# Kernel optimization log

Measured on AMD Instinct MI355X. Metric: run time of the kernel, lower is better.

The kernel has to match this reference:

```python
import jax, jax.numpy as jnp
import numpy as np

B, T, C = 4, 2048, 1024
H = 16
D = C // H  # head_dim = 64


def setup_inputs() -> dict:
    key = jax.random.key(0)
    k1, k2, k3 = jax.random.split(key, 3)
    x = jax.random.normal(k1, (B, T, C), dtype=jnp.float32)
    w_qkv = jax.random.normal(k2, (C, 3 * C), dtype=jnp.float32) * (C ** -0.5)
    b_qkv = jnp.zeros((3 * C,), dtype=jnp.float32)
    w_proj = jax.random.normal(k3, (C, C), dtype=jnp.float32) * (C ** -0.5)
    b_proj = jnp.zeros((C,), dtype=jnp.float32)
    return {"x": x, "w_qkv": w_qkv, "b_qkv": b_qkv, "w_proj": w_proj, "b_proj": b_proj}


def reference(x, w_qkv, b_qkv, w_proj, b_proj):
    # qkv projection: (B,T,C) -> (B,T,3,H,D) -> q,k,v each (B,H,T,D)
    qkv = (x @ w_qkv + b_qkv).reshape(B, T, 3, H, D)
    q, k, v = jnp.moveaxis(qkv, 2, 0)           # each (B, T, H, D)
    q = q.transpose(0, 2, 1, 3)                 # (B, H, T, D)
    k = k.transpose(0, 2, 1, 3)
    v = v.transpose(0, 2, 1, 3)

    scale = 1.0 / jnp.sqrt(jnp.float32(D))
    attn = jnp.einsum('bhqd,bhkd->bhqk', q, k) * scale  # (B,H,T,T)
    causal = jnp.tril(jnp.ones((T, T), dtype=bool))
    attn = jnp.where(causal[None, None], attn, -jnp.inf)
    attn = jax.nn.softmax(attn, axis=-1)
    # dropout p=0.0 (eval mode) -> identity
    out = jnp.einsum('bhqk,bhkd->bhqd', attn, v)        # (B,H,T,D)
    out = out.transpose(0, 2, 1, 3).reshape(B, T, C)
    return out @ w_proj + b_proj
```

## Files before the change

kernel.cpp:

```cpp
#include <hip/hip_runtime.h>
#include <hip/hip_bf16.h>


#define Bsz 4
#define Tsz 2048
#define Csz 1024
#define Hn  16
#define Dh  64

typedef unsigned short u16;
typedef __attribute__((ext_vector_type(8))) short bf16x8;
typedef __attribute__((ext_vector_type(4))) float f32x4;
typedef __attribute__((ext_vector_type(4))) unsigned int u32x4;
typedef __attribute__((ext_vector_type(2))) unsigned int u32x2;

__device__ __forceinline__ u16 f2b(float f) {
  __hip_bfloat16 h = __float2bfloat16(f);
  return *reinterpret_cast<u16*>(&h);
}

__device__ __forceinline__ unsigned pk2(float lo, float hi) {
  return __builtin_amdgcn_perm(__float_as_uint(hi) + 0x8000u,
                               __float_as_uint(lo) + 0x8000u, 0x07060302u);
}

#if __has_builtin(__builtin_amdgcn_exp2f)
#define EX2(x) __builtin_amdgcn_exp2f(x)
#else
#define EX2(x) exp2f(x)
#endif

__device__ __forceinline__ void gld_lds16(const void* g, void* lds) {
  __builtin_amdgcn_global_load_lds(
      (const __attribute__((address_space(1))) unsigned int*)g,
      (__attribute__((address_space(3))) unsigned int*)lds, 16, 0, 0);
}

__global__ __launch_bounds__(256) void prep(const float* __restrict__ x,
                                            u16* __restrict__ Xb,
                                            const float* __restrict__ w_qkv,
                                            u16* __restrict__ WqkvT,
                                            const float* __restrict__ w_proj,
                                            u16* __restrict__ WprojT) {
  const int bid = blockIdx.x;
  const int tid = threadIdx.x;
  if (bid < 4096) {
    size_t i = ((size_t)bid * 256 + tid) * 8;
    f32x4 a = *(const f32x4*)(x + i);
    f32x4 b = *(const f32x4*)(x + i + 4);
    u16 r[8];
#pragma unroll
    for (int j = 0; j < 4; ++j) { r[j] = f2b(a[j]); r[4 + j] = f2b(b[j]); }
    *(u32x4*)(Xb + i) = *(const u32x4*)r;
    return;
  }
  __shared__ u16 tile[64 * 66];
  const float* in;
  u16* out;
  int R, C, bx, by;
  int t = bid - 4096;
  if (t < 768) {
    in = w_qkv; out = WqkvT; R = 1024; C = 3072;
    bx = t & 15; by = t >> 4;
  } else {
    t -= 768;
    in = w_proj; out = WprojT; R = 1024; C = 1024;
    bx = t & 15; by = t >> 4;
  }
  const int r0 = bx * 64, c0 = by * 64;
#pragma unroll
  for (int i = 0; i < 16; ++i) {
    int idx = i * 256 + tid;
    int r = idx >> 6, c = idx & 63;
    tile[r * 66 + c] = f2b(in[(size_t)(r0 + r) * C + (c0 + c)]);
  }
  __syncthreads();
#pragma unroll
  for (int i = 0; i < 16; ++i) {
    int idx = i * 256 + tid;
    int c = idx >> 6, r = idx & 63;
    out[(size_t)(c0 + c) * R + (r0 + r)] = tile[r * 66 + c];
  }
}

__device__ __forceinline__ void gemm_tile_acc(const u16* __restrict__ A,
                                              const u16* __restrict__ Bt,
                                              int m0, int n0,
                                              u16* Als, u16* Bls,
                                              f32x4 acc[4][2]) {
  const int tid = threadIdx.x;
  const int w = tid >> 6, lane = tid & 63;
  const int wm = w & 1, wn = w >> 1;
  const int col = lane & 15, quad = lane >> 4;
#pragma unroll
  for (int mt = 0; mt < 4; ++mt)
#pragma unroll
    for (int nt = 0; nt < 2; ++nt)
      acc[mt][nt] = (f32x4){0.f, 0.f, 0.f, 0.f};

  const u16* asrc[2];
  const u16* bsrc[2];
#pragma unroll
  for (int c = 0; c < 2; ++c) {
    int slot = c * 512 + tid;
    int trow = slot >> 3, seg = slot & 7;
    size_t off = (size_t)trow * 1024 + (size_t)((seg ^ (trow & 7)) * 8);
    asrc[c] = A + (size_t)m0 * 1024 + off;
    bsrc[c] = Bt + (size_t)n0 * 1024 + off;
  }
  const int swz = col & 7;
  const int o0 = ((0 + quad) ^ swz) * 8;
  const int o1 = ((4 + quad) ^ swz) * 8;

#pragma unroll
  for (int c = 0; c < 2; ++c) {
    gld_lds16(asrc[c], (char*)Als + (size_t)(c * 512 + w * 64) * 16);
    gld_lds16(bsrc[c], (char*)Bls + (size_t)(c * 512 + w * 64) * 16);
    asrc[c] += 64; bsrc[c] += 64;
  }

  const int nkt = 1024 / 64;
  for (int t = 0; t < nkt; ++t) {
    asm volatile("s_waitcnt vmcnt(0)" ::: "memory");
    __builtin_amdgcn_s_barrier();
    __builtin_amdgcn_sched_barrier(0);
    const int cur = t & 1;
    if (t + 1 < nkt) {
      const int nxt = cur ^ 1;
      u16* Ad = Als + nxt * 8192;
      u16* Bd = Bls + nxt * 8192;
#pragma unroll
      for (int c = 0; c < 2; ++c) {
        gld_lds16(asrc[c], (char*)Ad + (size_t)(c * 512 + w * 64) * 16);
        gld_lds16(bsrc[c], (char*)Bd + (size_t)(c * 512 + w * 64) * 16);
        asrc[c] += 64; bsrc[c] += 64;
      }
    }
    const u16* Ac = Als + cur * 8192;
    const u16* Bc = Bls + cur * 8192;
    bf16x8 af[4][2], bfr[2][2];
#pragma unroll
    for (int mt = 0; mt < 4; ++mt) {
      const u16* r = Ac + (size_t)(wm * 64 + mt * 16 + col) * 64;
      af[mt][0] = *(const bf16x8*)(r + o0);
      af[mt][1] = *(const bf16x8*)(r + o1);
    }
#pragma unroll
    for (int nt = 0; nt < 2; ++nt) {
      const u16* r = Bc + (size_t)(wn * 32 + nt * 16 + col) * 64;
      bfr[nt][0] = *(const bf16x8*)(r + o0);
      bfr[nt][1] = *(const bf16x8*)(r + o1);
    }
#pragma unroll
    for (int kk = 0; kk < 2; ++kk)
#pragma unroll
      for (int mt = 0; mt < 4; ++mt)
#pragma unroll
        for (int nt = 0; nt < 2; ++nt)
          acc[mt][nt] = __builtin_amdgcn_mfma_f32_16x16x32_bf16(
              af[mt][kk], bfr[nt][kk], acc[mt][nt], 0, 0, 0);
  }
}

__global__ __launch_bounds__(512, 4) void gemm_qkv(const u16* __restrict__ X,
                                                   const u16* __restrict__ WT,
                                                   const float* __restrict__ bias,
                                                   u16* __restrict__ Q,
                                                   u16* __restrict__ Kc,
                                                   u16* __restrict__ Vt) {
  __shared__ __align__(16) u16 Als[2 * 128 * 64];
  __shared__ __align__(16) u16 Bls[2 * 128 * 64];
  f32x4 acc[4][2];
  const int m0 = blockIdx.x * 128, n0 = blockIdx.y * 128;
  gemm_tile_acc(X, WT, m0, n0, Als, Bls, acc);

  const float qscale = 0.18033688011112042f;
  const int tid = threadIdx.x;
  const int w = tid >> 6, lane = tid & 63;
  const int wm = w & 1, wn = w >> 1;
  const int col = lane & 15, quad = lane >> 4;
#pragma unroll
  for (int mt = 0; mt < 4; ++mt)
#pragma unroll
    for (int nt = 0; nt < 2; ++nt) {
      int n = n0 + wn * 32 + nt * 16 + col;
      int s = n >> 10, hh = (n >> 6) & (Hn - 1), d = n & 63;
      int mBase = m0 + wm * 64 + mt * 16 + quad * 4;
      int b = mBase >> 11, t0 = mBase & (Tsz - 1);
      if (s == 2) {
        u16 vals[4];
#pragma unroll
        for (int r = 0; r < 4; ++r) vals[r] = f2b(acc[mt][nt][r] + bias[n]);
        *(u32x2*)(Vt + ((size_t)(b * Hn + hh) * Dh + d) * Tsz + t0) =
            *(const u32x2*)vals;
      } else {
        const float scl = (s == 0) ? qscale : 1.f;
        u16* dst = (s == 0) ? Q : Kc;
#pragma unroll
        for (int r = 0; r < 4; ++r)
          dst[((size_t)(b * Hn + hh) * Tsz + (t0 + r)) * Dh + d] =
              f2b((acc[mt][nt][r] + bias[n]) * scl);
      }
    }
}

__global__ __launch_bounds__(512, 4) void gemm_proj(const u16* __restrict__ O,
                                                    const u16* __restrict__ WT,
                                                    const float* __restrict__ bias,
                                                    float* __restrict__ out) {
  __shared__ __align__(16) u16 Als[2 * 128 * 64];
  __shared__ __align__(16) u16 Bls[2 * 128 * 64];
  f32x4 acc[4][2];
  const int m0 = blockIdx.x * 128, n0 = blockIdx.y * 128;
  gemm_tile_acc(O, WT, m0, n0, Als, Bls, acc);

  const int tid = threadIdx.x;
  const int w = tid >> 6, lane = tid & 63;
  const int wm = w & 1, wn = w >> 1;
  const int col = lane & 15, quad = lane >> 4;
#pragma unroll
  for (int mt = 0; mt < 4; ++mt)
#pragma unroll
    for (int nt = 0; nt < 2; ++nt)
#pragma unroll
      for (int r = 0; r < 4; ++r) {
        int m = m0 + wm * 64 + mt * 16 + quad * 4 + r;
        int n = n0 + wn * 32 + nt * 16 + col;
        out[(size_t)m * Csz + n] = acc[mt][nt][r] + bias[n];
      }
}

__device__ __forceinline__ void attn_tile_stage(
    const u16* __restrict__ Kc, const u16* __restrict__ Vc,
    const bf16x8* aq, f32x4* oacc, float* lsum,
    bool domask, int rel, int qg, int col, int quad, int off0, int off1) {
  f32x4 sacc[4];
#pragma unroll
  for (int kt = 0; kt < 4; ++kt) sacc[kt] = (f32x4){0.f, 0.f, 0.f, 0.f};
#pragma unroll
  for (int ks = 0; ks < 2; ++ks)
#pragma unroll
    for (int kt = 0; kt < 4; ++kt) {
      bf16x8 bk = *(const bf16x8*)(&Kc[(kt * 16 + col) * 64 + (ks ? off1 : off0)]);
      sacc[kt] = __builtin_amdgcn_mfma_f32_16x16x32_bf16(bk, aq[ks],
                                                         sacc[kt], 0, 0, 0);
    }

  float e[4][4];
  if (domask) {
#pragma unroll
    for (int kt = 0; kt < 4; ++kt)
#pragma unroll
      for (int r = 0; r < 4; ++r) {
        int kl = rel + kt * 16 + quad * 4 + r;
        float p = (kl > qg) ? 0.f : EX2(sacc[kt][r]);
        lsum[kt] += p;
        e[kt][r] = p;
      }
  } else {
#pragma unroll
    for (int kt = 0; kt < 4; ++kt)
#pragma unroll
      for (int r = 0; r < 4; ++r) {
        float p = EX2(sacc[kt][r]);
        lsum[kt] += p;
        e[kt][r] = p;
      }
  }

#pragma unroll
  for (int ksg = 0; ksg < 2; ++ksg) {
    unsigned w00 = pk2(e[2 * ksg][0], e[2 * ksg][1]);
    unsigned w01 = pk2(e[2 * ksg][2], e[2 * ksg][3]);
    unsigned w10 = pk2(e[2 * ksg + 1][0], e[2 * ksg + 1][1]);
    unsigned w11 = pk2(e[2 * ksg + 1][2], e[2 * ksg + 1][3]);
    auto ra = __builtin_amdgcn_permlane32_swap(w00, w10, false, false);
    auto rb = __builtin_amdgcn_permlane32_swap(w01, w11, false, false);
    auto sa = __builtin_amdgcn_permlane16_swap(ra[0], ra[1], false, false);
    auto sb = __builtin_amdgcn_permlane16_swap(rb[0], rb[1], false, false);
    union { unsigned u[4]; bf16x8 v; } pf;
    pf.u[0] = sa[0]; pf.u[1] = sb[0]; pf.u[2] = sa[1]; pf.u[3] = sb[1];
#pragma unroll
    for (int dt = 0; dt < 4; ++dt) {
      bf16x8 bv = *(const bf16x8*)(&Vc[(dt * 16 + col) * 64 + (ksg ? off1 : off0)]);
      oacc[dt] = __builtin_amdgcn_mfma_f32_16x16x32_bf16(bv, pf.v,
                                                         oacc[dt], 0, 0, 0);
    }
  }
}

__global__ __launch_bounds__(512, 4) void attn(const u16* __restrict__ Q,
                                               const u16* __restrict__ Kg,
                                               const u16* __restrict__ Vt,
                                               u16* __restrict__ O) {
  __shared__ __align__(16) u16 Ks[3][64 * 64];
  __shared__ __align__(16) u16 Vs[3][64 * 64];

  const int d0 = blockIdx.x;
  const int xcd = d0 & 7;
  const int idx = d0 >> 3;
  const int bh = ((idx & 7) << 3) | xcd;
  const int a = idx >> 3;
  const int qlo = a, qhi = 15 - a;
  const int h = bh & (Hn - 1), b = bh >> 4;

  const int tid = threadIdx.x, w = tid >> 6, lane = tid & 63;
  const int col = lane & 15, quad = lane >> 4;
  const int qbl = qlo << 7, qbh = qhi << 7;

  const u16* Kbase = Kg + (size_t)bh * Tsz * Dh;
  const u16* Vbase = Vt + (size_t)bh * Dh * Tsz;

  const int trow = tid >> 3;
  const int xseg = ((tid & 7) ^ (trow & 7)) * 8;
  const size_t koff = (size_t)trow * 64 + xseg;
  const size_t voff = (size_t)trow * Tsz + xseg;
  const int swz = col & 7;
  const int off0 = ((0 + quad) ^ swz) << 3;
  const int off1 = ((4 + quad) ^ swz) << 3;

  bf16x8 aq_hi[2], aq_lo[2];
  {
    const u16* Qh = Q + ((size_t)bh * Tsz + qbh) * Dh;
    const u16* Ql = Q + ((size_t)bh * Tsz + qbl) * Dh;
#pragma unroll
    for (int ks = 0; ks < 2; ++ks) {
      aq_hi[ks] = *(const bf16x8*)(Qh + (size_t)(w * 16 + col) * Dh + ks * 32 + quad * 8);
      aq_lo[ks] = *(const bf16x8*)(Ql + (size_t)(w * 16 + col) * Dh + ks * 32 + quad * 8);
    }
  }
  asm volatile("s_waitcnt vmcnt(0)" ::: "memory");

  const int nst = 2 * qhi + 2;
  gld_lds16(Kbase + koff, &Ks[0][w * 512]);
  gld_lds16(Vbase + voff, &Vs[0][w * 512]);
  gld_lds16(Kbase + 4096 + koff, &Ks[1][w * 512]);
  gld_lds16(Vbase + 64 + voff, &Vs[1][w * 512]);

  f32x4 oacc_hi[4], oacc_lo[4];
#pragma unroll
  for (int dt = 0; dt < 4; ++dt) {
    oacc_hi[dt] = (f32x4){0.f, 0.f, 0.f, 0.f};
    oacc_lo[dt] = (f32x4){0.f, 0.f, 0.f, 0.f};
  }
  float lsum_hi[4] = {0.f, 0.f, 0.f, 0.f};
  float lsum_lo[4] = {0.f, 0.f, 0.f, 0.f};

  const u16* kdma = Kbase + 2 * 4096 + koff;
  const u16* vdma = Vbase + 2 * 64 + voff;

  const int qg = w * 16 + col;
  const int wge4 = (w >= 4) ? 1 : 0;
  const int smask_hi = 2 * qhi + wge4;
  const int smask_lo = 2 * qlo + wge4;
  const int lo_end = 2 * qlo + 1 + wge4;
  const int hi2 = 2 * qhi, lo2 = 2 * qlo;

  int cur = 0;
  for (int s = 0; s < nst; ++s) {
    if (s + 1 < nst) {
      asm volatile("s_waitcnt vmcnt(2)" ::: "memory");
    } else {
      asm volatile("s_waitcnt vmcnt(0)" ::: "memory");
    }
    __builtin_amdgcn_s_barrier();
    __builtin_amdgcn_sched_barrier(0);
    if (s + 2 < nst) {
      int pf = cur + 2; if (pf >= 3) pf -= 3;
      gld_lds16(kdma, &Ks[pf][w * 512]);
      gld_lds16(vdma, &Vs[pf][w * 512]);
      kdma += 4096;
      vdma += 64;
    }
    const u16* Kc = &Ks[cur][0];
    const u16* Vc = &Vs[cur][0];

    if (w >= 4 || s < nst - 1)
      attn_tile_stage(Kc, Vc, aq_hi, oacc_hi, lsum_hi,
                      s >= smask_hi, (s - hi2) * 64, qg, col, quad, off0, off1);
    if (s < lo_end)
      attn_tile_stage(Kc, Vc, aq_lo, oacc_lo, lsum_lo,
                      s >= smask_lo, (s - lo2) * 64, qg, col, quad, off0, off1);

    cur += 1; if (cur >= 3) cur = 0;
  }

  float vh = (lsum_hi[0] + lsum_hi[1]) + (lsum_hi[2] + lsum_hi[3]);
  vh += __shfl_xor(vh, 16);
  vh += __shfl_xor(vh, 32);
  const float invh = 1.0f / vh;
  float vl = (lsum_lo[0] + lsum_lo[1]) + (lsum_lo[2] + lsum_lo[3]);
  vl += __shfl_xor(vl, 16);
  vl += __shfl_xor(vl, 32);
  const float invl = 1.0f / vl;

  const int rgh = qbh + w * 16 + col;
  const int rgl = qbl + w * 16 + col;
  u16* OrowH = O + (((size_t)b * Tsz + rgh) * Hn + h) * Dh;
  u16* OrowL = O + (((size_t)b * Tsz + rgl) * Hn + h) * Dh;
#pragma unroll
  for (int dt = 0; dt < 4; ++dt) {
    u16 vh4[4], vl4[4];
#pragma unroll
    for (int r = 0; r < 4; ++r) {
      vh4[r] = f2b(oacc_hi[dt][r] * invh);
      vl4[r] = f2b(oacc_lo[dt][r] * invl);
    }
    *(u32x2*)(OrowH + dt * 16 + quad * 4) = *(const u32x2*)vh4;
    *(u32x2*)(OrowL + dt * 16 + quad * 4) = *(const u32x2*)vl4;
  }
}

extern "C" void kernel_launch(void* const* d_in, const int* in_sizes, int n_in,
                              void* d_out, int out_size, void* d_ws, size_t ws_size,
                              hipStream_t stream) {
  const float* x      = (const float*)d_in[0];
  const float* w_qkv  = (const float*)d_in[1];
  const float* b_qkv  = (const float*)d_in[2];
  const float* w_proj = (const float*)d_in[3];
  const float* b_proj = (const float*)d_in[4];
  float* out = (float*)d_out;

  u16* Xb     = (u16*)d_ws;
  u16* WqkvT  = Xb + (size_t)8192 * 1024;
  u16* WprojT = WqkvT + (size_t)3072 * 1024;
  u16* Qb     = WprojT + (size_t)1024 * 1024;
  u16* Kb     = Qb + (size_t)8192 * 1024;
  u16* Ob     = Kb + (size_t)8192 * 1024;
  u16* Vtb    = (u16*)d_out;

  prep<<<5120, 256, 0, stream>>>(x, Xb, w_qkv, WqkvT, w_proj, WprojT);
  gemm_qkv<<<dim3(64, 24), 512, 0, stream>>>(Xb, WqkvT, b_qkv, Qb, Kb, Vtb);
  attn<<<dim3(512), 512, 0, stream>>>(Qb, Kb, Vtb, Ob);
  gemm_proj<<<dim3(64, 8), 512, 0, stream>>>(Ob, WprojT, b_proj, out);
}
```

Measured before the change: 229.2 us.

## Use 256x256 block tiles for the QKV projection GEMM

Adds a new GEMM core that computes 256x256 output tiles per 512-thread block, with each wave holding an 8x4 grid of MFMA accumulators, and switches the QKV projection to it with a 32x12 grid. Larger tiles raise arithmetic intensity and cut global/LDS load traffic per FLOP. The cost is higher register and LDS use (64KB of double-buffered LDS), lower occupancy (launch bounds 2), and only 384 blocks, which is close to a single wave across the CUs and may leave some underused.

```diff
diff --git a/kernel.cpp b/kernel.cpp
--- a/kernel.cpp
+++ b/kernel.cpp
@@ -83,6 +83,122 @@
   }
 }
 
+__device__ __forceinline__ void gemm256_core(const u16* __restrict__ A,
+                                             const u16* __restrict__ Bt,
+                                             int m0, int n0,
+                                             u16* Als, u16* Bls,
+                                             f32x4 acc[8][4]) {
+  const int tid = threadIdx.x;
+  const int w = tid >> 6, lane = tid & 63;
+  const int wm = w & 1, wn = w >> 1;
+  const int col = lane & 15, quad = lane >> 4;
+#pragma unroll
+  for (int mt = 0; mt < 8; ++mt)
+#pragma unroll
+    for (int nt = 0; nt < 4; ++nt)
+      acc[mt][nt] = (f32x4){0.f, 0.f, 0.f, 0.f};
+
+  const u16* aP[4];
+  const u16* bP[4];
+#pragma unroll
+  for (int c = 0; c < 4; ++c) {
+    int slot = c * 512 + tid;
+    int trow = slot >> 3, seg = slot & 7;
+    size_t off = (size_t)trow * 1024 + (size_t)((seg ^ (trow & 7)) * 8);
+    aP[c] = A + (size_t)m0 * 1024 + off;
+    bP[c] = Bt + (size_t)n0 * 1024 + off;
+  }
+  const int swz = col & 7;
+  const int o0 = ((0 + quad) ^ swz) * 8;
+  const int o1 = ((4 + quad) ^ swz) * 8;
+
+#pragma unroll
+  for (int c = 0; c < 4; ++c) {
+    gld_lds16(aP[c], Als + c * 4096 + w * 512);
+    gld_lds16(bP[c], Bls + c * 4096 + w * 512);
+    aP[c] += 64; bP[c] += 64;
+  }
+
+  const int nkt = 1024 / 64;
+  for (int t = 0; t < nkt; ++t) {
+    asm volatile("s_waitcnt vmcnt(0)" ::: "memory");
+    __builtin_amdgcn_s_barrier();
+    __builtin_amdgcn_sched_barrier(0);
+    const int cur = t & 1;
+    if (t + 1 < nkt) {
+      const int nxt = cur ^ 1;
+      u16* Ad = Als + nxt * 16384;
+      u16* Bd = Bls + nxt * 16384;
+#pragma unroll
+      for (int c = 0; c < 4; ++c) {
+        gld_lds16(aP[c], Ad + c * 4096 + w * 512);
+        gld_lds16(bP[c], Bd + c * 4096 + w * 512);
+        aP[c] += 64; bP[c] += 64;
+      }
+    }
+    const u16* Ac = Als + cur * 16384;
+    const u16* Bc = Bls + cur * 16384;
+#pragma unroll
+    for (int ks = 0; ks < 2; ++ks) {
+      const int oo = ks ? o1 : o0;
+      bf16x8 bf[4];
+#pragma unroll
+      for (int nt = 0; nt < 4; ++nt)
+        bf[nt] = *(const bf16x8*)(Bc + (size_t)(wn * 64 + nt * 16 + col) * 64 + oo);
+#pragma unroll
+      for (int mt = 0; mt < 8; ++mt) {
+        bf16x8 af = *(const bf16x8*)(Ac + (size_t)(wm * 128 + mt * 16 + col) * 64 + oo);
+#pragma unroll
+        for (int nt = 0; nt < 4; ++nt)
+          acc[mt][nt] = __builtin_amdgcn_mfma_f32_16x16x32_bf16(af, bf[nt],
+                                                                acc[mt][nt], 0, 0, 0);
+      }
+    }
+  }
+}
+
+__global__ __launch_bounds__(512, 2) void gemm_qkv(const u16* __restrict__ X,
+                                                   const u16* __restrict__ WT,
+                                                   const float* __restrict__ bias,
+                                                   u16* __restrict__ Q,
+                                                   u16* __restrict__ Kc,
+                                                   u16* __restrict__ Vt) {
+  __shared__ __align__(16) u16 Als[2 * 256 * 64];
+  __shared__ __align__(16) u16 Bls[2 * 256 * 64];
+  f32x4 acc[8][4];
+  const int m0 = blockIdx.x * 256, n0 = blockIdx.y * 256;
+  gemm256_core(X, WT, m0, n0, Als, Bls, acc);
+
+  const float qscale = 0.18033688011112042f;
+  const int tid = threadIdx.x;
+  const int w = tid >> 6, lane = tid & 63;
+  const int wm = w & 1, wn = w >> 1;
+  const int col = lane & 15, quad = lane >> 4;
+#pragma unroll
+  for (int mt = 0; mt < 8; ++mt)
+#pragma unroll
+    for (int nt = 0; nt < 4; ++nt) {
+      int n = n0 + wn * 64 + nt * 16 + col;
+      int s = n >> 10, hh = (n >> 6) & (Hn - 1), d = n & 63;
+      int mBase = m0 + wm * 128 + mt * 16 + quad * 4;
+      int b = mBase >> 11, t0 = mBase & (Tsz - 1);
+      if (s == 2) {
+        u16 vals[4];
+#pragma unroll
+        for (int r = 0; r < 4; ++r) vals[r] = f2b(acc[mt][nt][r] + bias[n]);
+        *(u32x2*)(Vt + ((size_t)(b * Hn + hh) * Dh + d) * Tsz + t0) =
+            *(const u32x2*)vals;
+      } else {
+        const float scl = (s == 0) ? qscale : 1.f;
+        u16* dst = (s == 0) ? Q : Kc;
+#pragma unroll
+        for (int r = 0; r < 4; ++r)
+          dst[((size_t)(b * Hn + hh) * Tsz + (t0 + r)) * Dh + d] =
+              f2b((acc[mt][nt][r] + bias[n]) * scl);
+      }
+    }
+}
+
 __device__ __forceinline__ void gemm_tile_acc(const u16* __restrict__ A,
                                               const u16* __restrict__ Bt,
                                               int m0, int n0,
@@ -160,48 +276,6 @@
           acc[mt][nt] = __builtin_amdgcn_mfma_f32_16x16x32_bf16(
               af[mt][kk], bfr[nt][kk], acc[mt][nt], 0, 0, 0);
   }
-}
-
-__global__ __launch_bounds__(512, 4) void gemm_qkv(const u16* __restrict__ X,
-                                                   const u16* __restrict__ WT,
-                                                   const float* __restrict__ bias,
-                                                   u16* __restrict__ Q,
-                                                   u16* __restrict__ Kc,
-                                                   u16* __restrict__ Vt) {
-  __shared__ __align__(16) u16 Als[2 * 128 * 64];
-  __shared__ __align__(16) u16 Bls[2 * 128 * 64];
-  f32x4 acc[4][2];
-  const int m0 = blockIdx.x * 128, n0 = blockIdx.y * 128;
-  gemm_tile_acc(X, WT, m0, n0, Als, Bls, acc);
-
-  const float qscale = 0.18033688011112042f;
-  const int tid = threadIdx.x;
-  const int w = tid >> 6, lane = tid & 63;
-  const int wm = w & 1, wn = w >> 1;
-  const int col = lane & 15, quad = lane >> 4;
-#pragma unroll
-  for (int mt = 0; mt < 4; ++mt)
-#pragma unroll
-    for (int nt = 0; nt < 2; ++nt) {
-      int n = n0 + wn * 32 + nt * 16 + col;
-      int s = n >> 10, hh = (n >> 6) & (Hn - 1), d = n & 63;
-      int mBase = m0 + wm * 64 + mt * 16 + quad * 4;
-      int b = mBase >> 11, t0 = mBase & (Tsz - 1);
-      if (s == 2) {
-        u16 vals[4];
-#pragma unroll
-        for (int r = 0; r < 4; ++r) vals[r] = f2b(acc[mt][nt][r] + bias[n]);
-        *(u32x2*)(Vt + ((size_t)(b * Hn + hh) * Dh + d) * Tsz + t0) =
-            *(const u32x2*)vals;
-      } else {
-        const float scl = (s == 0) ? qscale : 1.f;
-        u16* dst = (s == 0) ? Q : Kc;
-#pragma unroll
-        for (int r = 0; r < 4; ++r)
-          dst[((size_t)(b * Hn + hh) * Tsz + (t0 + r)) * Dh + d] =
-              f2b((acc[mt][nt][r] + bias[n]) * scl);
-      }
-    }
 }
 
 __global__ __launch_bounds__(512, 4) void gemm_proj(const u16* __restrict__ O,
@@ -430,7 +504,7 @@
   u16* Vtb    = (u16*)d_out;
 
   prep<<<5120, 256, 0, stream>>>(x, Xb, w_qkv, WqkvT, w_proj, WprojT);
-  gemm_qkv<<<dim3(64, 24), 512, 0, stream>>>(Xb, WqkvT, b_qkv, Qb, Kb, Vtb);
+  gemm_qkv<<<dim3(32, 12), 512, 0, stream>>>(Xb, WqkvT, b_qkv, Qb, Kb, Vtb);
   attn<<<dim3(512), 512, 0, stream>>>(Qb, Kb, Vtb, Ob);
   gemm_proj<<<dim3(64, 8), 512, 0, stream>>>(Ob, WprojT, b_proj, out);
 }
```

Measured after the change: 243.4 us. +6.2%, slower.

## Load GEMM B operand directly from global into registers, drop B LDS staging

Applied to the files above, without the earlier changes.

The shared GEMM tile routine no longer stages the B (weight) tile through LDS. Each wave now reads its B fragments straight from global memory into registers every k-step. The change also halves shared memory per block and raises the launch-bounds occupancy hint from 4 to 6 for both QKV and projection GEMMs. This removes LDS traffic and footprint, but adds uncoalesced, unprefetched global loads on the critical path, and the wave pairs that share B columns now each fetch them separately.

```diff
diff --git a/kernel.cpp b/kernel.cpp
--- a/kernel.cpp
+++ b/kernel.cpp
@@ -86,7 +86,7 @@
 __device__ __forceinline__ void gemm_tile_acc(const u16* __restrict__ A,
                                               const u16* __restrict__ Bt,
                                               int m0, int n0,
-                                              u16* Als, u16* Bls,
+                                              u16* Als,
                                               f32x4 acc[4][2]) {
   const int tid = threadIdx.x;
   const int w = tid >> 6, lane = tid & 63;
@@ -99,24 +99,25 @@
       acc[mt][nt] = (f32x4){0.f, 0.f, 0.f, 0.f};
 
   const u16* asrc[2];
-  const u16* bsrc[2];
 #pragma unroll
   for (int c = 0; c < 2; ++c) {
     int slot = c * 512 + tid;
     int trow = slot >> 3, seg = slot & 7;
-    size_t off = (size_t)trow * 1024 + (size_t)((seg ^ (trow & 7)) * 8);
-    asrc[c] = A + (size_t)m0 * 1024 + off;
-    bsrc[c] = Bt + (size_t)n0 * 1024 + off;
+    asrc[c] = A + (size_t)m0 * 1024 + (size_t)trow * 1024 +
+              (size_t)((seg ^ (trow & 7)) * 8);
   }
   const int swz = col & 7;
   const int o0 = ((0 + quad) ^ swz) * 8;
   const int o1 = ((4 + quad) ^ swz) * 8;
 
+  const u16* bg[2];
+  bg[0] = Bt + (size_t)(n0 + wn * 32 + col) * 1024 + quad * 8;
+  bg[1] = Bt + (size_t)(n0 + wn * 32 + 16 + col) * 1024 + quad * 8;
+
 #pragma unroll
   for (int c = 0; c < 2; ++c) {
     gld_lds16(asrc[c], (char*)Als + (size_t)(c * 512 + w * 64) * 16);
-    gld_lds16(bsrc[c], (char*)Bls + (size_t)(c * 512 + w * 64) * 16);
-    asrc[c] += 64; bsrc[c] += 64;
+    asrc[c] += 64;
   }
 
   const int nkt = 1024 / 64;
@@ -128,17 +129,20 @@
     if (t + 1 < nkt) {
       const int nxt = cur ^ 1;
       u16* Ad = Als + nxt * 8192;
-      u16* Bd = Bls + nxt * 8192;
 #pragma unroll
       for (int c = 0; c < 2; ++c) {
         gld_lds16(asrc[c], (char*)Ad + (size_t)(c * 512 + w * 64) * 16);
-        gld_lds16(bsrc[c], (char*)Bd + (size_t)(c * 512 + w * 64) * 16);
-        asrc[c] += 64; bsrc[c] += 64;
+        asrc[c] += 64;
       }
     }
     const u16* Ac = Als + cur * 8192;
-    const u16* Bc = Bls + cur * 8192;
     bf16x8 af[4][2], bfr[2][2];
+    const int kofs = t * 64;
+#pragma unroll
+    for (int nt = 0; nt < 2; ++nt) {
+      bfr[nt][0] = *(const bf16x8*)(bg[nt] + kofs);
+      bfr[nt][1] = *(const bf16x8*)(bg[nt] + kofs + 32);
+    }
 #pragma unroll
     for (int mt = 0; mt < 4; ++mt) {
       const u16* r = Ac + (size_t)(wm * 64 + mt * 16 + col) * 64;
@@ -146,12 +150,6 @@
       af[mt][1] = *(const bf16x8*)(r + o1);
     }
 #pragma unroll
-    for (int nt = 0; nt < 2; ++nt) {
-      const u16* r = Bc + (size_t)(wn * 32 + nt * 16 + col) * 64;
-      bfr[nt][0] = *(const bf16x8*)(r + o0);
-      bfr[nt][1] = *(const bf16x8*)(r + o1);
-    }
-#pragma unroll
     for (int kk = 0; kk < 2; ++kk)
 #pragma unroll
       for (int mt = 0; mt < 4; ++mt)
@@ -162,17 +160,16 @@
   }
 }
 
-__global__ __launch_bounds__(512, 4) void gemm_qkv(const u16* __restrict__ X,
+__global__ __launch_bounds__(512, 6) void gemm_qkv(const u16* __restrict__ X,
                                                    const u16* __restrict__ WT,
                                                    const float* __restrict__ bias,
                                                    u16* __restrict__ Q,
                                                    u16* __restrict__ Kc,
                                                    u16* __restrict__ Vt) {
   __shared__ __align__(16) u16 Als[2 * 128 * 64];
-  __shared__ __align__(16) u16 Bls[2 * 128 * 64];
   f32x4 acc[4][2];
   const int m0 = blockIdx.x * 128, n0 = blockIdx.y * 128;
-  gemm_tile_acc(X, WT, m0, n0, Als, Bls, acc);
+  gemm_tile_acc(X, WT, m0, n0, Als, acc);
 
   const float qscale = 0.18033688011112042f;
   const int tid = threadIdx.x;
@@ -204,15 +201,14 @@
     }
 }
 
-__global__ __launch_bounds__(512, 4) void gemm_proj(const u16* __restrict__ O,
+__global__ __launch_bounds__(512, 6) void gemm_proj(const u16* __restrict__ O,
                                                     const u16* __restrict__ WT,
                                                     const float* __restrict__ bias,
                                                     float* __restrict__ out) {
   __shared__ __align__(16) u16 Als[2 * 128 * 64];
-  __shared__ __align__(16) u16 Bls[2 * 128 * 64];
   f32x4 acc[4][2];
   const int m0 = blockIdx.x * 128, n0 = blockIdx.y * 128;
-  gemm_tile_acc(O, WT, m0, n0, Als, Bls, acc);
+  gemm_tile_acc(O, WT, m0, n0, Als, acc);
 
   const int tid = threadIdx.x;
   const int w = tid >> 6, lane = tid & 63;
```

After: 294.3 us. 28.4% more time.
